# Optimization experiments

Measured on AMD Instinct MI355X. Metric: run time of the kernel, lower is better.

## Reference

```python
import jax, jax.numpy as jnp
import numpy as np

B, L, C = 2, 8192, 256
K, NLEV = 17, 4
HALF = K // 2


def setup_inputs() -> dict:
    key = jax.random.key(0)
    ks = jax.random.split(key, 10)
    s = 0.02
    return {
        "x": jax.random.normal(ks[0], (B, L, C), jnp.float32),
        "stem_w": jax.random.normal(ks[1], (C, C, 2), jnp.float32) * s,   # Conv1d (out,in,k)
        "stem_b": jax.random.normal(ks[2], (C,), jnp.float32) * s,
        "qkv_w": jax.random.normal(ks[3], (3 * C, C), jnp.float32) * s,
        "width_w": jax.random.normal(ks[4], (1, C), jnp.float32) * s,
        "width_b": jax.random.normal(ks[5], (1,), jnp.float32) * s,
        "out_w": jax.random.normal(ks[6], (C, C), jnp.float32) * s,
        "query": jax.random.normal(ks[7], (NLEV * C,), jnp.float32) * s,
        "film_w": jax.random.normal(ks[8], (2 * C, NLEV * C), jnp.float32) * s,
        "film_b": jax.random.normal(ks[9], (2 * C,), jnp.float32) * s,
    }


def _local_attn(h, qkv_w, width_w, width_b, out_w):
    # h: (b, l, c); 1D local windowed attention with learned sigmoid distance mask
    b, l, c = h.shape
    rel_dist = jnp.abs(jnp.arange(K, dtype=h.dtype) - HALF)  # (K,)
    max_dist = float(HALF)
    scale = c ** -0.5
    qkv = h @ qkv_w.T
    q, k, v = jnp.split(qkv, 3, axis=-1)
    width = jax.nn.sigmoid(h @ width_w.T + width_b) * max_dist + 0.5  # (b,l,1)
    k_pad = jnp.pad(k, ((0, 0), (HALF, HALF), (0, 0)))
    v_pad = jnp.pad(v, ((0, 0), (HALF, HALF), (0, 0)))
    idx = jnp.arange(l)[:, None] + jnp.arange(K)[None, :]  # (l,K) indices into padded seq
    k_win = k_pad[:, idx]  # (b,l,K,c)
    v_win = v_pad[:, idx]  # (b,l,K,c)
    scores = jnp.einsum('blc,blwc->blw', q, k_win) * scale
    soft_mask = jax.nn.sigmoid((width - rel_dist) * 5.0)  # (b,l,K)
    scores = scores - (1.0 - soft_mask) * 10000.0
    attn = jax.nn.softmax(scores, axis=-1)
    o = jnp.einsum('blw,blwc->blc', attn, v_win)
    return (o + v) @ out_w.T


def _forward(x, stem_w, stem_b, qkv_w, width_w, width_b, out_w, query, film_w, film_b):
    b, l, c = x.shape
    # stem conv: Conv1d(C, C, kernel=2, padding=1), then narrow to first l positions
    h = jnp.transpose(x, (0, 2, 1))  # (B,C,L)
    h = jax.lax.conv_general_dilated(h, stem_w, (1,), [(1, 1)],
                                     dimension_numbers=('NCH', 'OIH', 'NCH'))
    h = h[:, :, :l] + stem_b[None, :, None]
    h = jnp.transpose(h, (0, 2, 1))  # (B,L,C)
    levels = []
    for i in range(NLEV):
        h = _local_attn(h, qkv_w, width_w, width_b, out_w)
        levels.append(h)
        if i < NLEV - 1:  # avg_pool(kernel=2, stride=2)
            bl = h.shape[1]
            h = h.reshape(b, bl // 2, 2, c).mean(axis=2)
    # nearest upsample each coarser level back to L (factors are exact powers of 2)
    ups = [levels[0]]
    for lvl in levels[1:]:
        ups.append(jnp.repeat(lvl, l // lvl.shape[1], axis=1))
    concat = jnp.concatenate(ups, axis=-1)  # (B,L,NLEV*C)
    gattn = jax.nn.softmax(concat @ query, axis=-1)  # (B,L)
    global_ctx = jnp.einsum('bl,bld->bd', gattn, concat)  # (B,NLEV*C)
    film = global_ctx @ film_w.T + film_b  # (B,2C)
    scale_f, bias_f = jnp.split(film, 2, axis=-1)
    return levels[0] * (1.0 + scale_f[:, None, :]) + bias_f[:, None, :]


def reference(x, stem_w, stem_b, qkv_w, width_w, width_b, out_w, query, film_w, film_b):
    return _forward(x, stem_w, stem_b, qkv_w, width_w, width_b, out_w, query, film_w, film_b)
```

## Files before the change

### kernel.cpp

```cpp
#include <hip/hip_runtime.h>
#include <math.h>

#define L_SEQ 8192
#define B_SZ  2
#define CH    256
#define NLEV  4

typedef __attribute__((ext_vector_type(8))) short bf16x8;
typedef __attribute__((ext_vector_type(4))) float f32x4;

static __device__ __forceinline__ float sigmoidf_(float x) {
    return 1.0f / (1.0f + expf(-x));
}

static __device__ __forceinline__ float bf2f_(unsigned short u) {
    union { unsigned int ui; float f; } x;
    x.ui = ((unsigned int)u) << 16;
    return x.f;
}
static __device__ __forceinline__ unsigned short f2b_(float f) {
    union { float f; unsigned int u; } x;
    x.f = f;
    unsigned int lsb = (x.u >> 16) & 1u;
    unsigned int r = x.u + 0x7fffu + lsb;
    return (unsigned short)(r >> 16);
}
static __device__ __forceinline__ float4 ldb4_(const unsigned short* p) {
    ushort4 u = *(const ushort4*)p;
    return make_float4(bf2f_(u.x), bf2f_(u.y), bf2f_(u.z), bf2f_(u.w));
}

#define NPREP_BLOCKS 17409
__global__ __launch_bounds__(256) void prep_kernel(
    const float* __restrict__ x, const float* __restrict__ qkv_w,
    const float* __restrict__ out_w, const float* __restrict__ stem_w,
    unsigned short* __restrict__ x16g, unsigned short* __restrict__ qw16,
    unsigned short* __restrict__ sw16)
{
    __shared__ float owr[256];
    if (blockIdx.x >= NPREP_BLOCKS) {
        const int c = blockIdx.x - NPREP_BLOCKS, j = threadIdx.x;
        owr[j] = out_w[(size_t)c * 256 + j];
        __syncthreads();
        float acc = 0.0f;
        #pragma unroll 8
        for (int k = 0; k < 256; ++k)
            acc += owr[k] * qkv_w[(size_t)(512 + k) * 256 + j];
        qw16[(size_t)(512 + c) * 256 + j] = f2b_(acc);
        return;
    }
    int i = blockIdx.x * 256 + threadIdx.x;
    if (i < 256) { x16g[i] = 0; return; }
    i -= 256;
    if (i < 4194304) { x16g[256 + i] = f2b_(x[i]); return; }
    i -= 4194304;
    if (i < 131072) { qw16[i] = f2b_(qkv_w[i]); return; }
    i -= 131072;
    {
        int k = i & 511, nn = i >> 9;
        float v = (k < 256) ? stem_w[(size_t)nn * 512 + k * 2]
                            : stem_w[(size_t)nn * 512 + (k - 256) * 2 + 1];
        sw16[i] = f2b_(v);
    }
}

__global__ __launch_bounds__(256) void stem_gemm_bf16(
    const unsigned short* __restrict__ x16g, const unsigned short* __restrict__ W,
    unsigned short* __restrict__ outB, const float* __restrict__ bias)
{
    __shared__ unsigned short As[128 * 32];
    __shared__ unsigned short Bs[128 * 32];
    const int tid  = threadIdx.x;
    const int wave = tid >> 6;
    const int lane = tid & 63;
    const int bm = blockIdx.y * 128;
    const int bn = blockIdx.x * 128;
    const int wm = (wave & 1) * 64;
    const int wn = (wave >> 1) * 64;
    const int srow = lane >> 2;
    const int scol = (lane & 3) * 8;

    f32x4 acc[4][4] = {};

    for (int k0 = 0; k0 < 512; k0 += 32) {
        __syncthreads();
        #pragma unroll
        for (int c = 0; c < 2; ++c) {
            const int chunk = c * 4 + wave;
            const int row = bm + chunk * 16 + srow;
            const int t = row & (L_SEQ - 1);
            const unsigned short* ga;
            if (k0 < 256)
                ga = x16g + (t > 0 ? (size_t)row * 256 : 0) + k0 + scol;
            else
                ga = x16g + ((size_t)row + 1) * 256 + (k0 - 256) + scol;
            const unsigned short* gw = W + (size_t)(bn + chunk * 16 + srow) * 512 + k0 + scol;
            __builtin_amdgcn_global_load_lds(
                (const __attribute__((address_space(1))) void*)ga,
                (__attribute__((address_space(3))) void*)(As + chunk * 16 * 32),
                16, 0, 0);
            __builtin_amdgcn_global_load_lds(
                (const __attribute__((address_space(1))) void*)gw,
                (__attribute__((address_space(3))) void*)(Bs + chunk * 16 * 32),
                16, 0, 0);
        }
        __syncthreads();

        bf16x8 af[4], bf[4];
        const int fr = lane & 15;
        const int kk = (lane >> 4) * 8;
        #pragma unroll
        for (int i = 0; i < 4; ++i) {
            af[i] = *(const bf16x8*)(As + (wm + i * 16 + fr) * 32 + kk);
            bf[i] = *(const bf16x8*)(Bs + (wn + i * 16 + fr) * 32 + kk);
        }
        #pragma unroll
        for (int i = 0; i < 4; ++i)
            #pragma unroll
            for (int j = 0; j < 4; ++j)
                acc[i][j] = __builtin_amdgcn_mfma_f32_16x16x32_bf16(
                    af[i], bf[j], acc[i][j], 0, 0, 0);
    }

    const int cn = lane & 15;
    const int cr = (lane >> 4) * 4;
    #pragma unroll
    for (int i = 0; i < 4; ++i)
        #pragma unroll
        for (int r = 0; r < 4; ++r) {
            const int m = bm + wm + i * 16 + cr + r;
            #pragma unroll
            for (int j = 0; j < 4; ++j) {
                const int n = bn + wn + j * 16 + cn;
                outB[(size_t)m * CH + n] = f2b_(acc[i][j][r] + bias[n]);
            }
        }
}

__global__ __launch_bounds__(256) void gemm_bf16(
    const unsigned short* __restrict__ A, const unsigned short* __restrict__ W,
    unsigned short* __restrict__ outB, int M, int N, int Kd)
{
    __shared__ unsigned short As[128 * 32];
    __shared__ unsigned short Bs[128 * 32];
    const int tid  = threadIdx.x;
    const int wave = tid >> 6;
    const int lane = tid & 63;
    const int bm = blockIdx.y * 128;
    const int bn = blockIdx.x * 128;
    const int wm = (wave & 1) * 64;
    const int wn = (wave >> 1) * 64;
    const int srow = lane >> 2;
    const int scol = (lane & 3) * 8;

    f32x4 acc[4][4] = {};

    for (int k0 = 0; k0 < Kd; k0 += 32) {
        __syncthreads();
        #pragma unroll
        for (int c = 0; c < 2; ++c) {
            const int chunk = c * 4 + wave;
            const int row = chunk * 16 + srow;
            const unsigned short* ga = A + (size_t)(bm + row) * Kd + k0 + scol;
            const unsigned short* gw = W + (size_t)(bn + row) * Kd + k0 + scol;
            __builtin_amdgcn_global_load_lds(
                (const __attribute__((address_space(1))) void*)ga,
                (__attribute__((address_space(3))) void*)(As + chunk * 16 * 32),
                16, 0, 0);
            __builtin_amdgcn_global_load_lds(
                (const __attribute__((address_space(1))) void*)gw,
                (__attribute__((address_space(3))) void*)(Bs + chunk * 16 * 32),
                16, 0, 0);
        }
        __syncthreads();

        bf16x8 af[4], bf[4];
        const int fr = lane & 15;
        const int kk = (lane >> 4) * 8;
        #pragma unroll
        for (int i = 0; i < 4; ++i) {
            af[i] = *(const bf16x8*)(As + (wm + i * 16 + fr) * 32 + kk);
            bf[i] = *(const bf16x8*)(Bs + (wn + i * 16 + fr) * 32 + kk);
        }
        #pragma unroll
        for (int i = 0; i < 4; ++i)
            #pragma unroll
            for (int j = 0; j < 4; ++j)
                acc[i][j] = __builtin_amdgcn_mfma_f32_16x16x32_bf16(
                    af[i], bf[j], acc[i][j], 0, 0, 0);
    }

    const int cn = lane & 15;
    const int cr = (lane >> 4) * 4;
    #pragma unroll
    for (int i = 0; i < 4; ++i)
        #pragma unroll
        for (int r = 0; r < 4; ++r) {
            const int m = bm + wm + i * 16 + cr + r;
            const size_t rowoff = (size_t)m * N;
            #pragma unroll
            for (int j = 0; j < 4; ++j)
                outB[rowoff + bn + wn + j * 16 + cn] = f2b_(acc[i][j][r]);
        }
}

__global__ __launch_bounds__(256, 1) void attn_vp_kernel(
    const unsigned short* __restrict__ qkv, const unsigned short* __restrict__ h16,
    const float* __restrict__ ww, const float* __restrict__ wbp,
    unsigned short* __restrict__ l16o, unsigned short* __restrict__ dsB, int l)
{
    __shared__ __align__(16) unsigned short vt[256 * 88];
    __shared__ __align__(16) unsigned short pb[4 * 512];

    const int tid  = threadIdx.x;
    const int wave = tid >> 6;
    const int lane = tid & 63;
    const int q    = lane >> 4;
    const int n    = lane & 15;

    int bid = blockIdx.x;
    const int cpx = gridDim.x >> 3;
    bid = (bid & 7) * cpx + (bid >> 3);

    const int bps = l >> 6;
    const int b  = bid / bps;
    const int t0 = (bid % bps) << 6;
    const size_t seqbase = (size_t)b * l;
    const int row0 = t0 + wave * 16;

    bf16x8 hv[8];
    {
        const unsigned short* hrow = h16 + (seqbase + row0 + n) * 256 + q * 64;
        #pragma unroll
        for (int jj = 0; jj < 8; ++jj) hv[jj] = *(const bf16x8*)(hrow + jj * 8);
    }
    bf16x8 qf[8];
    {
        const unsigned short* qrow = qkv + (seqbase + row0 + n) * 768 + q * 8;
        #pragma unroll
        for (int kk = 0; kk < 8; ++kk) qf[kk] = *(const bf16x8*)(qrow + kk * 32);
    }
    bf16x8 bk[2][8];
    #pragma unroll
    for (int h = 0; h < 2; ++h) {
        const int grow = row0 - 8 + h * 16 + n;
        const bool ok = (grow >= 0 && grow < l);
        const unsigned short* kb = qkv + (seqbase + grow) * 768 + 256 + q * 8;
        #pragma unroll
        for (int kk = 0; kk < 8; ++kk) {
            bf16x8 z = {0, 0, 0, 0, 0, 0, 0, 0};
            bk[h][kk] = ok ? *(const bf16x8*)(kb + kk * 32) : z;
        }
    }
    bf16x8 vval[10];
    {
        const int r = tid & 15;
        const int ch0 = tid >> 4;
        #pragma unroll
        for (int p5 = 0; p5 < 5; ++p5)
            #pragma unroll
            for (int cc = 0; cc < 2; ++cc) {
                const int grow = t0 - 8 + p5 * 16 + r;
                bf16x8 val = {0, 0, 0, 0, 0, 0, 0, 0};
                if (grow >= 0 && grow < l)
                    val = *(const bf16x8*)(qkv + (seqbase + grow) * 768 + 512 +
                                           (cc * 16 + ch0) * 8);
                vval[p5 * 2 + cc] = val;
            }
    }
    __builtin_amdgcn_sched_barrier(0);

    float wdot = 0.0f;
    #pragma unroll
    for (int jj = 0; jj < 8; ++jj) {
        float4 wa = *((const float4*)(ww + q * 64 + jj * 8));
        float4 wc = *((const float4*)(ww + q * 64 + jj * 8 + 4));
        wdot += bf2f_((unsigned short)hv[jj][0]) * wa.x
              + bf2f_((unsigned short)hv[jj][1]) * wa.y
              + bf2f_((unsigned short)hv[jj][2]) * wa.z
              + bf2f_((unsigned short)hv[jj][3]) * wa.w
              + bf2f_((unsigned short)hv[jj][4]) * wc.x
              + bf2f_((unsigned short)hv[jj][5]) * wc.y
              + bf2f_((unsigned short)hv[jj][6]) * wc.z
              + bf2f_((unsigned short)hv[jj][7]) * wc.w;
    }
    wdot += __shfl_xor(wdot, 16, 64);
    wdot += __shfl_xor(wdot, 32, 64);
    const float w_n = sigmoidf_(wdot + wbp[0]) * 8.0f + 0.5f;

    f32x4 accS[2] = {};
    #pragma unroll
    for (int h = 0; h < 2; ++h)
        #pragma unroll
        for (int kk = 0; kk < 8; ++kk)
            accS[h] = __builtin_amdgcn_mfma_f32_16x16x32_bf16(
                qf[kk], bk[h][kk], accS[h], 0, 0, 0);

    float wd[4];
    #pragma unroll
    for (int r = 0; r < 4; ++r) wd[r] = __shfl(w_n, q * 4 + r, 64);

    float s[2][4];
    #pragma unroll
    for (int h = 0; h < 2; ++h)
        #pragma unroll
        for (int r = 0; r < 4; ++r) {
            int ii = q * 4 + r;
            int c  = h * 16 + n;
            int w  = c - ii;
            float dist = fabsf((float)w - 8.0f);
            float sm = sigmoidf_((wd[r] - dist) * 5.0f);
            float v = accS[h][r] * 0.0625f - (1.0f - sm) * 10000.0f;
            s[h][r] = (w >= 0 && w <= 16) ? v : -3.0e38f;
        }

    float mx[4], sum[4];
    #pragma unroll
    for (int r = 0; r < 4; ++r) mx[r] = fmaxf(s[0][r], s[1][r]);
    #pragma unroll
    for (int m = 1; m < 16; m <<= 1)
        #pragma unroll
        for (int r = 0; r < 4; ++r) mx[r] = fmaxf(mx[r], __shfl_xor(mx[r], m, 64));
    float e[2][4];
    #pragma unroll
    for (int h = 0; h < 2; ++h)
        #pragma unroll
        for (int r = 0; r < 4; ++r) e[h][r] = expf(s[h][r] - mx[r]);
    #pragma unroll
    for (int r = 0; r < 4; ++r) sum[r] = e[0][r] + e[1][r];
    #pragma unroll
    for (int m = 1; m < 16; m <<= 1)
        #pragma unroll
        for (int r = 0; r < 4; ++r) sum[r] += __shfl_xor(sum[r], m, 64);

    #pragma unroll
    for (int h = 0; h < 2; ++h)
        #pragma unroll
        for (int r = 0; r < 4; ++r) {
            int ii = q * 4 + r, c = h * 16 + n;
            float p = e[h][r] / sum[r];
            if (c == ii + 8) p += 1.0f;
            pb[wave * 512 + ii * 32 + c] = f2b_(p);
        }

    {
        const int r = tid & 15;
        const int ch0 = tid >> 4;
        #pragma unroll
        for (int p5 = 0; p5 < 5; ++p5)
            #pragma unroll
            for (int cc = 0; cc < 2; ++cc) {
                const int rr = p5 * 16 + r;
                const int chunk = cc * 16 + ch0;
                #pragma unroll
                for (int jj = 0; jj < 8; ++jj)
                    vt[(chunk * 8 + jj) * 88 + rr] =
                        (unsigned short)vval[p5 * 2 + cc][jj];
            }
    }

    __syncthreads();

    bf16x8 pf = *(const bf16x8*)(pb + wave * 512 + n * 32 + q * 8);
    const int rl = q * 4;
    const size_t gbase = seqbase + row0;
    #pragma unroll
    for (int ct = 0; ct < 16; ++ct) {
        bf16x8 vf = *(const bf16x8*)(vt + (ct * 16 + n) * 88 + wave * 16 + q * 8);
        f32x4 z = {};
        f32x4 o = __builtin_amdgcn_mfma_f32_16x16x32_bf16(pf, vf, z, 0, 0, 0);
        const int col = ct * 16 + n;
        float v0 = o[0], v1 = o[1], v2 = o[2], v3 = o[3];
        size_t r0 = (gbase + rl) * CH + col;
        l16o[r0]          = f2b_(v0);
        l16o[r0 + CH]     = f2b_(v1);
        l16o[r0 + 2 * CH] = f2b_(v2);
        l16o[r0 + 3 * CH] = f2b_(v3);
        if (dsB) {
            size_t d0 = ((gbase + rl) >> 1) * CH + col;
            dsB[d0]      = f2b_(0.5f * (v0 + v1));
            dsB[d0 + CH] = f2b_(0.5f * (v2 + v3));
        }
    }
}

__global__ __launch_bounds__(1024) void tail_ctx_kernel(
    const unsigned short* __restrict__ l0, const unsigned short* __restrict__ l1,
    const unsigned short* __restrict__ l2, const unsigned short* __restrict__ l3,
    const float* __restrict__ query, float* __restrict__ partials,
    float* __restrict__ denomP)
{
    __shared__ float eS[128];
    const int tid = threadIdx.x;
    const int chunk = blockIdx.x, b = blockIdx.y;
    const int t0 = chunk * 128;
    const unsigned short* levp[4] = {l0, l1, l2, l3};

    const int w = tid >> 6, lane = tid & 63;
    const int lev = lane >> 4, c0 = (lane & 15) * 16;
    const unsigned short* lpbase = levp[lev] + (size_t)b * (L_SEQ >> lev) * CH;
    const float* qp = query + lev * CH + c0;
    float4 q0 = *(const float4*)(qp);
    float4 q1 = *(const float4*)(qp + 4);
    float4 q2 = *(const float4*)(qp + 8);
    float4 q3 = *(const float4*)(qp + 12);
    #pragma unroll
    for (int j = 0; j < 8; ++j) {
        int t = t0 + w * 8 + j;
        const unsigned short* p = lpbase + (size_t)(t >> lev) * CH + c0;
        float4 h0 = ldb4_(p), h1 = ldb4_(p + 4), h2 = ldb4_(p + 8), h3 = ldb4_(p + 12);
        float part = h0.x * q0.x + h0.y * q0.y + h0.z * q0.z + h0.w * q0.w
                   + h1.x * q1.x + h1.y * q1.y + h1.z * q1.z + h1.w * q1.w
                   + h2.x * q2.x + h2.y * q2.y + h2.z * q2.z + h2.w * q2.w
                   + h3.x * q3.x + h3.y * q3.y + h3.z * q3.z + h3.w * q3.w;
        #pragma unroll
        for (int m = 1; m < 64; m <<= 1) part += __shfl_xor(part, m, 64);
        if (lane == 0) eS[w * 8 + j] = expf(part);
    }
    __syncthreads();

    if (tid == 0) {
        float ds = 0.0f;
        #pragma unroll 8
        for (int i = 0; i < 128; ++i) ds += eS[i];
        denomP[b * 64 + chunk] = ds;
    }

    const int dlev = tid >> 8, c = tid & 255;
    const unsigned short* lp = levp[dlev] + (size_t)b * (L_SEQ >> dlev) * CH;
    float acc = 0.0f;
    #pragma unroll 4
    for (int t = t0; t < t0 + 128; ++t)
        acc += eS[t - t0] * bf2f_(lp[(size_t)(t >> dlev) * CH + c]);
    partials[(size_t)(b * 64 + chunk) * 1024 + tid] = acc;
}

__global__ __launch_bounds__(256) void ctx_reduce_kernel(
    const float* __restrict__ partials, const float* __restrict__ denomP,
    float* __restrict__ ctx)
{
    const int b = blockIdx.y;
    const int d = blockIdx.x * 256 + threadIdx.x;
    float acc = 0.0f;
    #pragma unroll
    for (int c = 0; c < 64; ++c) acc += partials[(size_t)(b * 64 + c) * 1024 + d];
    float den = 0.0f;
    #pragma unroll
    for (int c = 0; c < 64; ++c) den += denomP[b * 64 + c];
    ctx[b * 1024 + d] = acc / den;
}

__global__ __launch_bounds__(256) void film_kernel(
    const float* __restrict__ ctx, const float* __restrict__ fw,
    const float* __restrict__ fb, float* __restrict__ film)
{
    const int lane = threadIdx.x & 63;
    const int j = blockIdx.x * 4 + (threadIdx.x >> 6);
    float acc0 = 0.0f, acc1 = 0.0f;
    #pragma unroll
    for (int r = 0; r < 4; ++r) {
        float4 w4 = *((const float4*)(fw + (size_t)j * 1024 + r * 256) + lane);
        float4 c0 = *((const float4*)(ctx + r * 256) + lane);
        float4 c1 = *((const float4*)(ctx + 1024 + r * 256) + lane);
        acc0 += w4.x * c0.x + w4.y * c0.y + w4.z * c0.z + w4.w * c0.w;
        acc1 += w4.x * c1.x + w4.y * c1.y + w4.z * c1.z + w4.w * c1.w;
    }
    #pragma unroll
    for (int m = 1; m < 64; m <<= 1) {
        acc0 += __shfl_xor(acc0, m, 64);
        acc1 += __shfl_xor(acc1, m, 64);
    }
    if (lane == 0) {
        float b = fb[j];
        film[j] = acc0 + b;
        film[512 + j] = acc1 + b;
    }
}

__global__ void final_kernel(const unsigned short* __restrict__ lev0,
                             const float* __restrict__ film,
                             float* __restrict__ out)
{
    size_t n4 = ((size_t)blockIdx.x * 256 + threadIdx.x) * 4;
    int c = (int)(n4 & (CH - 1));
    int b = (int)(n4 >> 21);
    float4 h = ldb4_(lev0 + n4);
    const float* fs = film + b * 512;
    float4 o;
    o.x = h.x * (1.0f + fs[c + 0]) + fs[256 + c + 0];
    o.y = h.y * (1.0f + fs[c + 1]) + fs[256 + c + 1];
    o.z = h.z * (1.0f + fs[c + 2]) + fs[256 + c + 2];
    o.w = h.w * (1.0f + fs[c + 3]) + fs[256 + c + 3];
    *(float4*)(out + n4) = o;
}

extern "C" void kernel_launch(void* const* d_in, const int* in_sizes, int n_in,
                              void* d_out, int out_size, void* d_ws, size_t ws_size,
                              hipStream_t stream) {
    const float* x       = (const float*)d_in[0];
    const float* stem_w  = (const float*)d_in[1];
    const float* stem_b  = (const float*)d_in[2];
    const float* qkv_w   = (const float*)d_in[3];
    const float* width_w = (const float*)d_in[4];
    const float* width_b = (const float*)d_in[5];
    const float* out_w   = (const float*)d_in[6];
    const float* query   = (const float*)d_in[7];
    const float* film_w  = (const float*)d_in[8];
    const float* film_b  = (const float*)d_in[9];
    float* out = (float*)d_out;
    float* ws  = (float*)d_ws;

    float* partials = ws;
    float* denomP   = partials + 131072;
    float* ctx      = denomP + 128;
    float* film     = ctx + 2048;
    unsigned short* x16g  = (unsigned short*)(film + 1024);
    unsigned short* h16_0 = x16g + 4194560;
    unsigned short* h16_1 = h16_0 + 4194304;
    unsigned short* h16_2 = h16_1 + 2097152;
    unsigned short* h16_3 = h16_2 + 1048576;
    unsigned short* qkv16 = h16_3 + 524288;
    unsigned short* ov16  = qkv16 + 12582912;
    unsigned short* l16_0 = ov16 + 4194304;
    unsigned short* l16_1 = l16_0 + 4194304;
    unsigned short* l16_2 = l16_1 + 2097152;
    unsigned short* l16_3 = l16_2 + 1048576;
    unsigned short* qw16  = l16_3 + 524288;
    unsigned short* ow16  = qw16 + 196608;
    unsigned short* sw16  = ow16 + 65536;
    unsigned short* h16[4]  = {h16_0, h16_1, h16_2, h16_3};
    unsigned short* l16[4]  = {l16_0, l16_1, l16_2, l16_3};
    (void)ov16; (void)ow16;

    prep_kernel<<<NPREP_BLOCKS + 256, 256, 0, stream>>>(
        x, qkv_w, out_w, stem_w, x16g, qw16, sw16);

    stem_gemm_bf16<<<dim3(CH / 128, B_SZ * L_SEQ / 128), 256, 0, stream>>>(
        x16g, sw16, h16_0, stem_b);

    for (int i = 0; i < NLEV; ++i) {
        const int l = L_SEQ >> i;
        const int M = B_SZ * l;
        gemm_bf16<<<dim3(768 / 128, M / 128), 256, 0, stream>>>(
            h16[i], qw16, qkv16, M, 768, CH);
        attn_vp_kernel<<<M / 64, 256, 0, stream>>>(
            qkv16, h16[i], width_w, width_b,
            l16[i], (i < NLEV - 1) ? h16[i + 1] : nullptr, l);
    }

    tail_ctx_kernel<<<dim3(64, B_SZ), 1024, 0, stream>>>(
        l16_0, l16_1, l16_2, l16_3, query, partials, denomP);
    ctx_reduce_kernel<<<dim3(4, B_SZ), 256, 0, stream>>>(partials, denomP, ctx);
    film_kernel<<<128, 256, 0, stream>>>(ctx, film_w, film_b, film);
    final_kernel<<<(B_SZ * L_SEQ * CH) / 1024, 256, 0, stream>>>(l16_0, film, out);
}
```

Measured before the change: 249.0 us.

## Split attention kernel across 8 waves with K-split scores and channel-split PV

Measured after the change: 241.3 us. -3.1%, faster.

```diff
diff --git a/kernel.cpp b/kernel.cpp
--- a/kernel.cpp
+++ b/kernel.cpp
@@ -204,17 +204,21 @@
         }
 }
 
-__global__ __launch_bounds__(256, 1) void attn_vp_kernel(
+__global__ __launch_bounds__(512, 2) void attn_vp_kernel(
     const unsigned short* __restrict__ qkv, const unsigned short* __restrict__ h16,
     const float* __restrict__ ww, const float* __restrict__ wbp,
     unsigned short* __restrict__ l16o, unsigned short* __restrict__ dsB, int l)
 {
     __shared__ __align__(16) unsigned short vt[256 * 88];
+    __shared__ __align__(16) float sp1[4 * 2 * 64 * 4];
     __shared__ __align__(16) unsigned short pb[4 * 512];
+    __shared__ float ws1[64];
 
     const int tid  = threadIdx.x;
     const int wave = tid >> 6;
     const int lane = tid & 63;
+    const int rt   = wave & 3;
+    const int half = wave >> 2;
     const int q    = lane >> 4;
     const int n    = lane & 15;
 
@@ -226,55 +230,53 @@
     const int b  = bid / bps;
     const int t0 = (bid % bps) << 6;
     const size_t seqbase = (size_t)b * l;
-    const int row0 = t0 + wave * 16;
-
-    bf16x8 hv[8];
+    const int row0 = t0 + rt * 16;
+    const int kc0  = half * 128;
+
+    bf16x8 hv[4];
     {
-        const unsigned short* hrow = h16 + (seqbase + row0 + n) * 256 + q * 64;
-        #pragma unroll
-        for (int jj = 0; jj < 8; ++jj) hv[jj] = *(const bf16x8*)(hrow + jj * 8);
-    }
-    bf16x8 qf[8];
+        const unsigned short* hrow = h16 + (seqbase + row0 + n) * 256 + kc0 + q * 32;
+        #pragma unroll
+        for (int jj = 0; jj < 4; ++jj) hv[jj] = *(const bf16x8*)(hrow + jj * 8);
+    }
+    bf16x8 qf[4];
     {
-        const unsigned short* qrow = qkv + (seqbase + row0 + n) * 768 + q * 8;
-        #pragma unroll
-        for (int kk = 0; kk < 8; ++kk) qf[kk] = *(const bf16x8*)(qrow + kk * 32);
-    }
-    bf16x8 bk[2][8];
+        const unsigned short* qrow = qkv + (seqbase + row0 + n) * 768 + kc0 + q * 8;
+        #pragma unroll
+        for (int j = 0; j < 4; ++j) qf[j] = *(const bf16x8*)(qrow + j * 32);
+    }
+    bf16x8 bk[2][4];
     #pragma unroll
     for (int h = 0; h < 2; ++h) {
         const int grow = row0 - 8 + h * 16 + n;
         const bool ok = (grow >= 0 && grow < l);
-        const unsigned short* kb = qkv + (seqbase + grow) * 768 + 256 + q * 8;
-        #pragma unroll
-        for (int kk = 0; kk < 8; ++kk) {
+        const unsigned short* kb = qkv + (seqbase + grow) * 768 + 256 + kc0 + q * 8;
+        #pragma unroll
+        for (int j = 0; j < 4; ++j) {
             bf16x8 z = {0, 0, 0, 0, 0, 0, 0, 0};
-            bk[h][kk] = ok ? *(const bf16x8*)(kb + kk * 32) : z;
-        }
-    }
-    bf16x8 vval[10];
-    {
-        const int r = tid & 15;
-        const int ch0 = tid >> 4;
-        #pragma unroll
-        for (int p5 = 0; p5 < 5; ++p5)
-            #pragma unroll
-            for (int cc = 0; cc < 2; ++cc) {
-                const int grow = t0 - 8 + p5 * 16 + r;
-                bf16x8 val = {0, 0, 0, 0, 0, 0, 0, 0};
-                if (grow >= 0 && grow < l)
-                    val = *(const bf16x8*)(qkv + (seqbase + grow) * 768 + 512 +
-                                           (cc * 16 + ch0) * 8);
-                vval[p5 * 2 + cc] = val;
-            }
-    }
+            bk[h][j] = ok ? *(const bf16x8*)(kb + j * 32) : z;
+        }
+    }
+    bf16x8 vv[8];
+    #pragma unroll
+    for (int c = 0; c < 4; ++c)
+        #pragma unroll
+        for (int i = 0; i < 2; ++i) {
+            const int r = i * 64 + lane;
+            const int grow = t0 - 8 + r;
+            bf16x8 val = {0, 0, 0, 0, 0, 0, 0, 0};
+            if (r < 80 && grow >= 0 && grow < l)
+                val = *(const bf16x8*)(qkv + (seqbase + grow) * 768 + 512 +
+                                       (wave * 4 + c) * 8);
+            vv[c * 2 + i] = val;
+        }
     __builtin_amdgcn_sched_barrier(0);
 
     float wdot = 0.0f;
     #pragma unroll
-    for (int jj = 0; jj < 8; ++jj) {
-        float4 wa = *((const float4*)(ww + q * 64 + jj * 8));
-        float4 wc = *((const float4*)(ww + q * 64 + jj * 8 + 4));
+    for (int jj = 0; jj < 4; ++jj) {
+        float4 wa = *((const float4*)(ww + kc0 + q * 32 + jj * 8));
+        float4 wc = *((const float4*)(ww + kc0 + q * 32 + jj * 8 + 4));
         wdot += bf2f_((unsigned short)hv[jj][0]) * wa.x
               + bf2f_((unsigned short)hv[jj][1]) * wa.y
               + bf2f_((unsigned short)hv[jj][2]) * wa.z
@@ -286,87 +288,98 @@
     }
     wdot += __shfl_xor(wdot, 16, 64);
     wdot += __shfl_xor(wdot, 32, 64);
-    const float w_n = sigmoidf_(wdot + wbp[0]) * 8.0f + 0.5f;
+    if (half == 1 && q == 0) ws1[rt * 16 + n] = wdot;
 
     f32x4 accS[2] = {};
     #pragma unroll
     for (int h = 0; h < 2; ++h)
         #pragma unroll
-        for (int kk = 0; kk < 8; ++kk)
+        for (int j = 0; j < 4; ++j)
             accS[h] = __builtin_amdgcn_mfma_f32_16x16x32_bf16(
-                qf[kk], bk[h][kk], accS[h], 0, 0, 0);
-
-    float wd[4];
-    #pragma unroll
-    for (int r = 0; r < 4; ++r) wd[r] = __shfl(w_n, q * 4 + r, 64);
-
-    float s[2][4];
-    #pragma unroll
-    for (int h = 0; h < 2; ++h)
-        #pragma unroll
-        for (int r = 0; r < 4; ++r) {
-            int ii = q * 4 + r;
-            int c  = h * 16 + n;
-            int w  = c - ii;
-            float dist = fabsf((float)w - 8.0f);
-            float sm = sigmoidf_((wd[r] - dist) * 5.0f);
-            float v = accS[h][r] * 0.0625f - (1.0f - sm) * 10000.0f;
-            s[h][r] = (w >= 0 && w <= 16) ? v : -3.0e38f;
-        }
-
-    float mx[4], sum[4];
-    #pragma unroll
-    for (int r = 0; r < 4; ++r) mx[r] = fmaxf(s[0][r], s[1][r]);
-    #pragma unroll
-    for (int m = 1; m < 16; m <<= 1)
-        #pragma unroll
-        for (int r = 0; r < 4; ++r) mx[r] = fmaxf(mx[r], __shfl_xor(mx[r], m, 64));
-    float e[2][4];
-    #pragma unroll
-    for (int h = 0; h < 2; ++h)
-        #pragma unroll
-        for (int r = 0; r < 4; ++r) e[h][r] = expf(s[h][r] - mx[r]);
-    #pragma unroll
-    for (int r = 0; r < 4; ++r) sum[r] = e[0][r] + e[1][r];
-    #pragma unroll
-    for (int m = 1; m < 16; m <<= 1)
-        #pragma unroll
-        for (int r = 0; r < 4; ++r) sum[r] += __shfl_xor(sum[r], m, 64);
-
-    #pragma unroll
-    for (int h = 0; h < 2; ++h)
-        #pragma unroll
-        for (int r = 0; r < 4; ++r) {
-            int ii = q * 4 + r, c = h * 16 + n;
-            float p = e[h][r] / sum[r];
-            if (c == ii + 8) p += 1.0f;
-            pb[wave * 512 + ii * 32 + c] = f2b_(p);
-        }
-
-    {
-        const int r = tid & 15;
-        const int ch0 = tid >> 4;
-        #pragma unroll
-        for (int p5 = 0; p5 < 5; ++p5)
-            #pragma unroll
-            for (int cc = 0; cc < 2; ++cc) {
-                const int rr = p5 * 16 + r;
-                const int chunk = cc * 16 + ch0;
+                qf[j], bk[h][j], accS[h], 0, 0, 0);
+
+    if (half == 1) {
+        *(f32x4*)(sp1 + ((rt * 2 + 0) * 64 + lane) * 4) = accS[0];
+        *(f32x4*)(sp1 + ((rt * 2 + 1) * 64 + lane) * 4) = accS[1];
+    }
+
+    #pragma unroll
+    for (int c = 0; c < 4; ++c)
+        #pragma unroll
+        for (int i = 0; i < 2; ++i) {
+            const int r = i * 64 + lane;
+            if (i == 0 || lane < 16) {
                 #pragma unroll
                 for (int jj = 0; jj < 8; ++jj)
-                    vt[(chunk * 8 + jj) * 88 + rr] =
-                        (unsigned short)vval[p5 * 2 + cc][jj];
+                    vt[((wave * 4 + c) * 8 + jj) * 88 + r] =
+                        (unsigned short)vv[c * 2 + i][jj];
             }
-    }
+        }
 
     __syncthreads();
 
-    bf16x8 pf = *(const bf16x8*)(pb + wave * 512 + n * 32 + q * 8);
+    if (half == 0) {
+        accS[0] += *(const f32x4*)(sp1 + ((rt * 2 + 0) * 64 + lane) * 4);
+        accS[1] += *(const f32x4*)(sp1 + ((rt * 2 + 1) * 64 + lane) * 4);
+        const float w_n = sigmoidf_(wdot + ws1[rt * 16 + n] + wbp[0]) * 8.0f + 0.5f;
+
+        float wd[4];
+        #pragma unroll
+        for (int r = 0; r < 4; ++r) wd[r] = __shfl(w_n, q * 4 + r, 64);
+
+        float s[2][4];
+        #pragma unroll
+        for (int h = 0; h < 2; ++h)
+            #pragma unroll
+            for (int r = 0; r < 4; ++r) {
+                int ii = q * 4 + r;
+                int c  = h * 16 + n;
+                int w  = c - ii;
+                float dist = fabsf((float)w - 8.0f);
+                float sm = sigmoidf_((wd[r] - dist) * 5.0f);
+                float v = accS[h][r] * 0.0625f - (1.0f - sm) * 10000.0f;
+                s[h][r] = (w >= 0 && w <= 16) ? v : -3.0e38f;
+            }
+
+        float mx[4], sum[4];
+        #pragma unroll
+        for (int r = 0; r < 4; ++r) mx[r] = fmaxf(s[0][r], s[1][r]);
+        #pragma unroll
+        for (int m = 1; m < 16; m <<= 1)
+            #pragma unroll
+            for (int r = 0; r < 4; ++r) mx[r] = fmaxf(mx[r], __shfl_xor(mx[r], m, 64));
+        float e[2][4];
+        #pragma unroll
+        for (int h = 0; h < 2; ++h)
+            #pragma unroll
+            for (int r = 0; r < 4; ++r) e[h][r] = expf(s[h][r] - mx[r]);
+        #pragma unroll
+        for (int r = 0; r < 4; ++r) sum[r] = e[0][r] + e[1][r];
+        #pragma unroll
+        for (int m = 1; m < 16; m <<= 1)
+            #pragma unroll
+            for (int r = 0; r < 4; ++r) sum[r] += __shfl_xor(sum[r], m, 64);
+
+        #pragma unroll
+        for (int h = 0; h < 2; ++h)
+            #pragma unroll
+            for (int r = 0; r < 4; ++r) {
+                int ii = q * 4 + r, c = h * 16 + n;
+                float p = e[h][r] / sum[r];
+                if (c == ii + 8) p += 1.0f;
+                pb[rt * 512 + ii * 32 + c] = f2b_(p);
+            }
+    }
+
+    __syncthreads();
+
+    bf16x8 pf = *(const bf16x8*)(pb + rt * 512 + n * 32 + q * 8);
     const int rl = q * 4;
     const size_t gbase = seqbase + row0;
     #pragma unroll
-    for (int ct = 0; ct < 16; ++ct) {
-        bf16x8 vf = *(const bf16x8*)(vt + (ct * 16 + n) * 88 + wave * 16 + q * 8);
+    for (int c = 0; c < 8; ++c) {
+        const int ct = half * 8 + c;
+        bf16x8 vf = *(const bf16x8*)(vt + (ct * 16 + n) * 88 + rt * 16 + q * 8);
         f32x4 z = {};
         f32x4 o = __builtin_amdgcn_mfma_f32_16x16x32_bf16(pf, vf, z, 0, 0, 0);
         const int col = ct * 16 + n;
@@ -543,7 +556,7 @@
         const int M = B_SZ * l;
         gemm_bf16<<<dim3(768 / 128, M / 128), 256, 0, stream>>>(
             h16[i], qw16, qkv16, M, 768, CH);
-        attn_vp_kernel<<<M / 64, 256, 0, stream>>>(
+        attn_vp_kernel<<<M / 64, 512, 0, stream>>>(
             qkv16, h16[i], width_w, width_b,
             l16[i], (i < NLEV - 1) ? h16[i + 1] : nullptr, l);
     }
```
